# Kernel tuning notes

Hardware: AMD Instinct MI355X
Metric: run time of the kernel (lower is better)

The kernel has to match this reference:

```python
import jax, jax.numpy as jnp
import numpy as np

B, H, W, DIM, HEADS = 8, 128, 128, 256, 8
LH, LW = 8, 8
HD = DIM // HEADS
SCALE = HD ** -0.5
WS = LH * LW  # window size (tokens per window)


def setup_inputs() -> dict:
    key = jax.random.key(0)
    k1, k2, k3 = jax.random.split(key, 3)
    qkv = jax.random.normal(k1, (3, B, H * W, DIM), jnp.float32)
    lepe_w = jax.random.normal(k2, (DIM, 1, 3, 3), jnp.float32) * 0.1  # depthwise conv weight
    lepe_b = jax.random.normal(k3, (DIM,), jnp.float32) * 0.1
    return {"qkv": qkv, "lepe_w": lepe_w, "lepe_b": lepe_b}


def _to_local(x):
    # [B, L, C] -> [B*nH*nW, heads, LH*LW, head_dim]  (window partition)
    Bb, L, C = x.shape
    x = x.reshape(Bb, H // LH, LH, W // LW, LW, C).transpose(0, 1, 3, 2, 4, 5)
    x = x.reshape(-1, WS, HEADS, HD).transpose(0, 2, 1, 3)
    return x


def reference(qkv, lepe_w, lepe_b):
    q, k, v = qkv[0], qkv[1], qkv[2]
    Bb, L, C = q.shape
    q = _to_local(q) * SCALE            # [nWin, h, ws, d]
    k = _to_local(k)                    # [nWin, h, ws, d]
    # v windows in NCHW for depthwise LePE conv: [nWin, C, LH, LW]
    vw = v.reshape(Bb, H // LH, LH, W // LW, LW, C).transpose(0, 1, 3, 5, 2, 4)
    vw = vw.reshape(-1, C, LH, LW)
    lepe = jax.lax.conv_general_dilated(
        vw, lepe_w, window_strides=(1, 1), padding='SAME',
        feature_group_count=C,
        dimension_numbers=('NCHW', 'OIHW', 'NCHW')) + lepe_b[None, :, None, None]
    lepe = lepe.reshape(-1, HEADS, HD, WS).transpose(0, 1, 3, 2)   # [nWin, h, ws, d]
    vloc = vw.reshape(-1, HEADS, HD, WS).transpose(0, 1, 3, 2)     # [nWin, h, ws, d]
    attn = jax.nn.softmax(jnp.einsum('whqd,whkd->whqk', q, k), axis=-1)
    x = jnp.einsum('whqk,whkd->whqd', attn, vloc) + lepe           # [nWin, h, ws, d]
    # window merge back to [B, L, C]
    x = x.transpose(0, 2, 1, 3).reshape(-1, WS, C)
    x = x.reshape(Bb, H // LH, W // LW, LH, LW, C).transpose(0, 1, 3, 2, 4, 5)
    x = x.reshape(Bb, H * W, C)
    return x, q
```

## Files before the change

### kernel.cpp

```cpp
#include <hip/hip_runtime.h>
#include <hip/hip_bf16.h>


#define SCALE_F 0.17677669529663687f

typedef __attribute__((ext_vector_type(8))) short bf16x8;
typedef __attribute__((ext_vector_type(4))) float f32x4;

static __device__ __forceinline__ unsigned short f2bf(float f) {
    unsigned int u = __builtin_bit_cast(unsigned int, f);
    u += 0x7fffu + ((u >> 16) & 1u);
    return (unsigned short)(u >> 16);
}
static __device__ __forceinline__ float bf2f(unsigned short s) {
    unsigned int u = ((unsigned int)s) << 16;
    return __builtin_bit_cast(float, u);
}

__global__ __launch_bounds__(256) void lepe_attn_kernel(
    const float* __restrict__ qkv,
    const float* __restrict__ lw,
    const float* __restrict__ lb,
    float* __restrict__ out)
{
    const int bid  = blockIdx.x;
    const int head = bid & 7;
    const int win  = bid >> 3;
    const int ww   = win & 15;
    const int wh   = (win >> 4) & 15;
    const int b    = win >> 8;
    const int t    = threadIdx.x;

    __shared__ __align__(16) short q_hi[64][40];
    __shared__ __align__(16) short q_lo[64][40];
    __shared__ __align__(16) short k_hi[64][40];
    __shared__ __align__(16) short k_lo[64][40];
    __shared__ __align__(16) short v_t[32][72];
    __shared__ __align__(16) short P_lds[64][72];
    __shared__ float w_s[288];
    __shared__ float b_s[32];

    const float* Qp = qkv;
    const float* Kp = qkv + (size_t)33554432;
    const float* Vp = qkv + (size_t)67108864;
    float* xout = out;
    float* qout = out + (size_t)33554432;

    for (int i = t; i < 288; i += 256) w_s[i] = lw[head * 288 + i];
    if (t < 32) b_s[t] = lb[head * 32 + t];

    #pragma unroll
    for (int u = 0; u < 2; ++u) {
        const int idx = t + u * 256;
        const int s   = idx >> 3;
        const int d4  = idx & 7;
        const int row = wh * 8 + (s >> 3);
        const int col = ww * 8 + (s & 7);
        const size_t goff = ((size_t)(b * 16384 + row * 128 + col)) * 256
                          + head * 32 + d4 * 4;

        float4 fq = *(const float4*)(Qp + goff);
        fq.x *= SCALE_F; fq.y *= SCALE_F; fq.z *= SCALE_F; fq.w *= SCALE_F;
        *(float4*)(qout + ((size_t)bid * 64 + s) * 32 + d4 * 4) = fq;
        {
            unsigned short h0 = f2bf(fq.x), h1 = f2bf(fq.y),
                           h2 = f2bf(fq.z), h3 = f2bf(fq.w);
            unsigned short l0 = f2bf(fq.x - bf2f(h0)), l1 = f2bf(fq.y - bf2f(h1)),
                           l2 = f2bf(fq.z - bf2f(h2)), l3 = f2bf(fq.w - bf2f(h3));
            uint2 hp, lp;
            hp.x = (unsigned)h0 | ((unsigned)h1 << 16);
            hp.y = (unsigned)h2 | ((unsigned)h3 << 16);
            lp.x = (unsigned)l0 | ((unsigned)l1 << 16);
            lp.y = (unsigned)l2 | ((unsigned)l3 << 16);
            *(uint2*)&q_hi[s][d4 * 4] = hp;
            *(uint2*)&q_lo[s][d4 * 4] = lp;
        }
        {
            float4 fk = *(const float4*)(Kp + goff);
            unsigned short h0 = f2bf(fk.x), h1 = f2bf(fk.y),
                           h2 = f2bf(fk.z), h3 = f2bf(fk.w);
            unsigned short l0 = f2bf(fk.x - bf2f(h0)), l1 = f2bf(fk.y - bf2f(h1)),
                           l2 = f2bf(fk.z - bf2f(h2)), l3 = f2bf(fk.w - bf2f(h3));
            uint2 hp, lp;
            hp.x = (unsigned)h0 | ((unsigned)h1 << 16);
            hp.y = (unsigned)h2 | ((unsigned)h3 << 16);
            lp.x = (unsigned)l0 | ((unsigned)l1 << 16);
            lp.y = (unsigned)l2 | ((unsigned)l3 << 16);
            *(uint2*)&k_hi[s][d4 * 4] = hp;
            *(uint2*)&k_lo[s][d4 * 4] = lp;
        }
        {
            float4 fv = *(const float4*)(Vp + goff);
            const int sp = ((s & 15) << 2) | (s >> 4);
            v_t[d4 * 4 + 0][sp] = (short)f2bf(fv.x);
            v_t[d4 * 4 + 1][sp] = (short)f2bf(fv.y);
            v_t[d4 * 4 + 2][sp] = (short)f2bf(fv.z);
            v_t[d4 * 4 + 3][sp] = (short)f2bf(fv.w);
        }
    }
    __syncthreads();

    const int lane = t & 63;
    const int wid  = t >> 6;
    const int c    = lane & 15;
    const int g    = lane >> 4;
    const int i0   = wid * 16;

    bf16x8 aqh = *(const bf16x8*)&q_hi[i0 + c][g * 8];
    bf16x8 aql = *(const bf16x8*)&q_lo[i0 + c][g * 8];

    f32x4 sacc[4];
    #pragma unroll
    for (int jt = 0; jt < 4; ++jt) {
        bf16x8 bkh = *(const bf16x8*)&k_hi[jt * 16 + c][g * 8];
        bf16x8 bkl = *(const bf16x8*)&k_lo[jt * 16 + c][g * 8];
        f32x4 acc = {0.f, 0.f, 0.f, 0.f};
        acc = __builtin_amdgcn_mfma_f32_16x16x32_bf16(aqh, bkh, acc, 0, 0, 0);
        acc = __builtin_amdgcn_mfma_f32_16x16x32_bf16(aql, bkh, acc, 0, 0, 0);
        acc = __builtin_amdgcn_mfma_f32_16x16x32_bf16(aqh, bkl, acc, 0, 0, 0);
        sacc[jt] = acc;
    }

    float mx[4] = {-3.0e38f, -3.0e38f, -3.0e38f, -3.0e38f};
    #pragma unroll
    for (int jt = 0; jt < 4; ++jt)
        #pragma unroll
        for (int r = 0; r < 4; ++r)
            mx[r] = fmaxf(mx[r], sacc[jt][r]);
    #pragma unroll
    for (int r = 0; r < 4; ++r) {
        mx[r] = fmaxf(mx[r], __shfl_xor(mx[r], 1));
        mx[r] = fmaxf(mx[r], __shfl_xor(mx[r], 2));
        mx[r] = fmaxf(mx[r], __shfl_xor(mx[r], 4));
        mx[r] = fmaxf(mx[r], __shfl_xor(mx[r], 8));
    }
    float p[4][4];
    float sm[4] = {0.f, 0.f, 0.f, 0.f};
    #pragma unroll
    for (int jt = 0; jt < 4; ++jt)
        #pragma unroll
        for (int r = 0; r < 4; ++r) {
            p[jt][r] = __expf(sacc[jt][r] - mx[r]);
            sm[r] += p[jt][r];
        }
    #pragma unroll
    for (int r = 0; r < 4; ++r) {
        sm[r] += __shfl_xor(sm[r], 1);
        sm[r] += __shfl_xor(sm[r], 2);
        sm[r] += __shfl_xor(sm[r], 4);
        sm[r] += __shfl_xor(sm[r], 8);
    }
    #pragma unroll
    for (int r = 0; r < 4; ++r) {
        const float inv = 1.0f / sm[r];
        unsigned short b0 = f2bf(p[0][r] * inv);
        unsigned short b1 = f2bf(p[1][r] * inv);
        unsigned short b2 = f2bf(p[2][r] * inv);
        unsigned short b3 = f2bf(p[3][r] * inv);
        uint2 pk;
        pk.x = (unsigned)b0 | ((unsigned)b1 << 16);
        pk.y = (unsigned)b2 | ((unsigned)b3 << 16);
        *(uint2*)&P_lds[i0 + 4 * g + r][4 * c] = pk;
    }
    __syncthreads();

    f32x4 o0 = {0.f, 0.f, 0.f, 0.f};
    f32x4 o1 = {0.f, 0.f, 0.f, 0.f};
    #pragma unroll
    for (int ks = 0; ks < 2; ++ks) {
        bf16x8 pa  = *(const bf16x8*)&P_lds[i0 + c][ks * 32 + g * 8];
        bf16x8 vb0 = *(const bf16x8*)&v_t[c][ks * 32 + g * 8];
        bf16x8 vb1 = *(const bf16x8*)&v_t[16 + c][ks * 32 + g * 8];
        o0 = __builtin_amdgcn_mfma_f32_16x16x32_bf16(pa, vb0, o0, 0, 0, 0);
        o1 = __builtin_amdgcn_mfma_f32_16x16x32_bf16(pa, vb1, o1, 0, 0, 0);
    }
    __syncthreads();

    {
        const int td = t & 31;
        const int lh = t >> 5;
        float wv[9];
        #pragma unroll
        for (int k = 0; k < 9; ++k) wv[k] = w_s[td * 9 + k];
        float rv[3][8];
        #pragma unroll
        for (int dy = 0; dy < 3; ++dy) {
            const int r2 = lh + dy - 1;
            #pragma unroll
            for (int x = 0; x < 8; ++x) {
                if (r2 >= 0 && r2 < 8) {
                    const int s  = r2 * 8 + x;
                    const int sp = ((s & 15) << 2) | (s >> 4);
                    rv[dy][x] = bf2f((unsigned short)v_t[td][sp]);
                } else {
                    rv[dy][x] = 0.f;
                }
            }
        }
        float* lepe = (float*)P_lds;
        #pragma unroll
        for (int lwp = 0; lwp < 8; ++lwp) {
            float acc = b_s[td];
            #pragma unroll
            for (int dy = 0; dy < 3; ++dy)
                #pragma unroll
                for (int dx = 0; dx < 3; ++dx) {
                    const int x = lwp + dx - 1;
                    if (x >= 0 && x < 8) acc += wv[dy * 3 + dx] * rv[dy][x];
                }
            lepe[(lh * 8 + lwp) * 36 + td] = acc;
        }
    }
    __syncthreads();

    {
        const float* lepe = (const float*)P_lds;
        #pragma unroll
        for (int r = 0; r < 4; ++r) {
            const int s   = i0 + 4 * g + r;
            const int row = wh * 8 + (s >> 3);
            const int col = ww * 8 + (s & 7);
            float* xo = xout + ((size_t)(b * 16384 + row * 128 + col)) * 256
                      + head * 32;
            xo[c]      = o0[r] + lepe[s * 36 + c];
            xo[16 + c] = o1[r] + lepe[s * 36 + 16 + c];
        }
    }
}

extern "C" void kernel_launch(void* const* d_in, const int* in_sizes, int n_in,
                              void* d_out, int out_size, void* d_ws, size_t ws_size,
                              hipStream_t stream) {
    (void)in_sizes; (void)n_in; (void)out_size; (void)d_ws; (void)ws_size;
    const float* qkv = (const float*)d_in[0];
    const float* lw  = (const float*)d_in[1];
    const float* lb  = (const float*)d_in[2];
    float* out = (float*)d_out;
    lepe_attn_kernel<<<dim3(16384), dim3(256), 0, stream>>>(qkv, lw, lb, out);
}
```

Baseline: 153.6 us.

## Keep softmax probabilities in registers and fuse LePE conv into attention output

QK^T is computed transposed (K as the A operand), so each lane holds a full query column and softmax reductions need only two cross-lane shuffles. The normalized probabilities are packed straight into MFMA A-operand registers, which removes the P round trip through LDS and two barriers. The depthwise conv is computed per lane in the MFMA output layout from a new row-major V copy and added to the accumulators, removing the final LDS staging and barriers. The hi/lo split now truncates instead of rounding, occupancy is hinted at 5 blocks per CU, and the V^T column permutation is changed to match the new P layout. This adds register pressure and a second V store in LDS.

```diff
diff --git a/kernel.cpp b/kernel.cpp
--- a/kernel.cpp
+++ b/kernel.cpp
@@ -1,23 +1,35 @@
 #include <hip/hip_runtime.h>
-#include <hip/hip_bf16.h>
 
 
 #define SCALE_F 0.17677669529663687f
 
 typedef __attribute__((ext_vector_type(8))) short bf16x8;
 typedef __attribute__((ext_vector_type(4))) float f32x4;
+typedef __attribute__((ext_vector_type(4))) unsigned int u32x4;
 
 static __device__ __forceinline__ unsigned short f2bf(float f) {
-    unsigned int u = __builtin_bit_cast(unsigned int, f);
+    unsigned u = __builtin_bit_cast(unsigned, f);
     u += 0x7fffu + ((u >> 16) & 1u);
     return (unsigned short)(u >> 16);
 }
 static __device__ __forceinline__ float bf2f(unsigned short s) {
-    unsigned int u = ((unsigned int)s) << 16;
+    unsigned u = ((unsigned)s) << 16;
     return __builtin_bit_cast(float, u);
 }
-
-__global__ __launch_bounds__(256) void lepe_attn_kernel(
+static __device__ __forceinline__ void split2(float a, float b,
+                                              unsigned &hi, unsigned &lo) {
+    unsigned ua = __builtin_bit_cast(unsigned, a);
+    unsigned ub = __builtin_bit_cast(unsigned, b);
+    unsigned ha = ua & 0xffff0000u;
+    unsigned hb = ub & 0xffff0000u;
+    float ra = a - __builtin_bit_cast(float, ha);
+    float rb = b - __builtin_bit_cast(float, hb);
+    hi = (ha >> 16) | hb;
+    lo = (__builtin_bit_cast(unsigned, ra) >> 16)
+       | (__builtin_bit_cast(unsigned, rb) & 0xffff0000u);
+}
+
+__global__ __launch_bounds__(256, 5) void lepe_attn_kernel(
     const float* __restrict__ qkv,
     const float* __restrict__ lw,
     const float* __restrict__ lb,
@@ -36,7 +48,7 @@
     __shared__ __align__(16) short k_hi[64][40];
     __shared__ __align__(16) short k_lo[64][40];
     __shared__ __align__(16) short v_t[32][72];
-    __shared__ __align__(16) short P_lds[64][72];
+    __shared__ __align__(16) short v_lin[64][36];
     __shared__ float w_s[288];
     __shared__ float b_s[32];
 
@@ -60,43 +72,35 @@
                           + head * 32 + d4 * 4;
 
         float4 fq = *(const float4*)(Qp + goff);
+        float4 fk = *(const float4*)(Kp + goff);
+        float4 fv = *(const float4*)(Vp + goff);
+
         fq.x *= SCALE_F; fq.y *= SCALE_F; fq.z *= SCALE_F; fq.w *= SCALE_F;
         *(float4*)(qout + ((size_t)bid * 64 + s) * 32 + d4 * 4) = fq;
-        {
-            unsigned short h0 = f2bf(fq.x), h1 = f2bf(fq.y),
-                           h2 = f2bf(fq.z), h3 = f2bf(fq.w);
-            unsigned short l0 = f2bf(fq.x - bf2f(h0)), l1 = f2bf(fq.y - bf2f(h1)),
-                           l2 = f2bf(fq.z - bf2f(h2)), l3 = f2bf(fq.w - bf2f(h3));
-            uint2 hp, lp;
-            hp.x = (unsigned)h0 | ((unsigned)h1 << 16);
-            hp.y = (unsigned)h2 | ((unsigned)h3 << 16);
-            lp.x = (unsigned)l0 | ((unsigned)l1 << 16);
-            lp.y = (unsigned)l2 | ((unsigned)l3 << 16);
-            *(uint2*)&q_hi[s][d4 * 4] = hp;
-            *(uint2*)&q_lo[s][d4 * 4] = lp;
-        }
-        {
-            float4 fk = *(const float4*)(Kp + goff);
-            unsigned short h0 = f2bf(fk.x), h1 = f2bf(fk.y),
-                           h2 = f2bf(fk.z), h3 = f2bf(fk.w);
-            unsigned short l0 = f2bf(fk.x - bf2f(h0)), l1 = f2bf(fk.y - bf2f(h1)),
-                           l2 = f2bf(fk.z - bf2f(h2)), l3 = f2bf(fk.w - bf2f(h3));
-            uint2 hp, lp;
-            hp.x = (unsigned)h0 | ((unsigned)h1 << 16);
-            hp.y = (unsigned)h2 | ((unsigned)h3 << 16);
-            lp.x = (unsigned)l0 | ((unsigned)l1 << 16);
-            lp.y = (unsigned)l2 | ((unsigned)l3 << 16);
-            *(uint2*)&k_hi[s][d4 * 4] = hp;
-            *(uint2*)&k_lo[s][d4 * 4] = lp;
-        }
-        {
-            float4 fv = *(const float4*)(Vp + goff);
-            const int sp = ((s & 15) << 2) | (s >> 4);
-            v_t[d4 * 4 + 0][sp] = (short)f2bf(fv.x);
-            v_t[d4 * 4 + 1][sp] = (short)f2bf(fv.y);
-            v_t[d4 * 4 + 2][sp] = (short)f2bf(fv.z);
-            v_t[d4 * 4 + 3][sp] = (short)f2bf(fv.w);
-        }
+
+        uint2 hp, lp;
+        split2(fq.x, fq.y, hp.x, lp.x);
+        split2(fq.z, fq.w, hp.y, lp.y);
+        *(uint2*)&q_hi[s][d4 * 4] = hp;
+        *(uint2*)&q_lo[s][d4 * 4] = lp;
+
+        split2(fk.x, fk.y, hp.x, lp.x);
+        split2(fk.z, fk.w, hp.y, lp.y);
+        *(uint2*)&k_hi[s][d4 * 4] = hp;
+        *(uint2*)&k_lo[s][d4 * 4] = lp;
+
+        const unsigned short b0 = f2bf(fv.x), b1 = f2bf(fv.y),
+                             b2 = f2bf(fv.z), b3 = f2bf(fv.w);
+        uint2 vp;
+        vp.x = (unsigned)b0 | ((unsigned)b1 << 16);
+        vp.y = (unsigned)b2 | ((unsigned)b3 << 16);
+        *(uint2*)&v_lin[s][d4 * 4] = vp;
+        const int sp = ((s >> 1) & 1) * 32 + ((s >> 2) & 3) * 8
+                     + (s & 1) * 4 + (s >> 4);
+        v_t[d4 * 4 + 0][sp] = (short)b0;
+        v_t[d4 * 4 + 1][sp] = (short)b1;
+        v_t[d4 * 4 + 2][sp] = (short)b2;
+        v_t[d4 * 4 + 3][sp] = (short)b3;
     }
     __syncthreads();
 
@@ -106,125 +110,113 @@
     const int g    = lane >> 4;
     const int i0   = wid * 16;
 
-    bf16x8 aqh = *(const bf16x8*)&q_hi[i0 + c][g * 8];
-    bf16x8 aql = *(const bf16x8*)&q_lo[i0 + c][g * 8];
-
+    const bf16x8 bqh = *(const bf16x8*)&q_hi[i0 + c][g * 8];
+    const bf16x8 bql = *(const bf16x8*)&q_lo[i0 + c][g * 8];
     f32x4 sacc[4];
     #pragma unroll
     for (int jt = 0; jt < 4; ++jt) {
-        bf16x8 bkh = *(const bf16x8*)&k_hi[jt * 16 + c][g * 8];
-        bf16x8 bkl = *(const bf16x8*)&k_lo[jt * 16 + c][g * 8];
+        const bf16x8 akh = *(const bf16x8*)&k_hi[jt * 16 + c][g * 8];
+        const bf16x8 akl = *(const bf16x8*)&k_lo[jt * 16 + c][g * 8];
         f32x4 acc = {0.f, 0.f, 0.f, 0.f};
-        acc = __builtin_amdgcn_mfma_f32_16x16x32_bf16(aqh, bkh, acc, 0, 0, 0);
-        acc = __builtin_amdgcn_mfma_f32_16x16x32_bf16(aql, bkh, acc, 0, 0, 0);
-        acc = __builtin_amdgcn_mfma_f32_16x16x32_bf16(aqh, bkl, acc, 0, 0, 0);
+        acc = __builtin_amdgcn_mfma_f32_16x16x32_bf16(akh, bqh, acc, 0, 0, 0);
+        acc = __builtin_amdgcn_mfma_f32_16x16x32_bf16(akl, bqh, acc, 0, 0, 0);
+        acc = __builtin_amdgcn_mfma_f32_16x16x32_bf16(akh, bql, acc, 0, 0, 0);
         sacc[jt] = acc;
     }
 
-    float mx[4] = {-3.0e38f, -3.0e38f, -3.0e38f, -3.0e38f};
+    float mx = -3.0e38f;
     #pragma unroll
     for (int jt = 0; jt < 4; ++jt)
         #pragma unroll
         for (int r = 0; r < 4; ++r)
-            mx[r] = fmaxf(mx[r], sacc[jt][r]);
+            mx = fmaxf(mx, sacc[jt][r]);
+    mx = fmaxf(mx, __shfl_xor(mx, 16));
+    mx = fmaxf(mx, __shfl_xor(mx, 32));
+
+    float p[4][4];
+    float sm = 0.f;
+    #pragma unroll
+    for (int jt = 0; jt < 4; ++jt)
+        #pragma unroll
+        for (int r = 0; r < 4; ++r) {
+            p[jt][r] = __expf(sacc[jt][r] - mx);
+            sm += p[jt][r];
+        }
+    sm += __shfl_xor(sm, 16);
+    sm += __shfl_xor(sm, 32);
+    const float inv = 1.0f / sm;
+
+    unsigned dwA[4], dwB[4];
     #pragma unroll
     for (int r = 0; r < 4; ++r) {
-        mx[r] = fmaxf(mx[r], __shfl_xor(mx[r], 1));
-        mx[r] = fmaxf(mx[r], __shfl_xor(mx[r], 2));
-        mx[r] = fmaxf(mx[r], __shfl_xor(mx[r], 4));
-        mx[r] = fmaxf(mx[r], __shfl_xor(mx[r], 8));
-    }
-    float p[4][4];
-    float sm[4] = {0.f, 0.f, 0.f, 0.f};
-    #pragma unroll
-    for (int jt = 0; jt < 4; ++jt)
-        #pragma unroll
-        for (int r = 0; r < 4; ++r) {
-            p[jt][r] = __expf(sacc[jt][r] - mx[r]);
-            sm[r] += p[jt][r];
-        }
-    #pragma unroll
-    for (int r = 0; r < 4; ++r) {
-        sm[r] += __shfl_xor(sm[r], 1);
-        sm[r] += __shfl_xor(sm[r], 2);
-        sm[r] += __shfl_xor(sm[r], 4);
-        sm[r] += __shfl_xor(sm[r], 8);
-    }
-    #pragma unroll
-    for (int r = 0; r < 4; ++r) {
-        const float inv = 1.0f / sm[r];
-        unsigned short b0 = f2bf(p[0][r] * inv);
-        unsigned short b1 = f2bf(p[1][r] * inv);
-        unsigned short b2 = f2bf(p[2][r] * inv);
-        unsigned short b3 = f2bf(p[3][r] * inv);
-        uint2 pk;
-        pk.x = (unsigned)b0 | ((unsigned)b1 << 16);
-        pk.y = (unsigned)b2 | ((unsigned)b3 << 16);
-        *(uint2*)&P_lds[i0 + 4 * g + r][4 * c] = pk;
-    }
-    __syncthreads();
+        dwA[r] = (unsigned)f2bf(p[0][r] * inv)
+               | ((unsigned)f2bf(p[1][r] * inv) << 16);
+        dwB[r] = (unsigned)f2bf(p[2][r] * inv)
+               | ((unsigned)f2bf(p[3][r] * inv) << 16);
+    }
+    const u32x4 w0 = {dwA[0], dwB[0], dwA[1], dwB[1]};
+    const u32x4 w1 = {dwA[2], dwB[2], dwA[3], dwB[3]};
+    const bf16x8 pa0 = __builtin_bit_cast(bf16x8, w0);
+    const bf16x8 pa1 = __builtin_bit_cast(bf16x8, w1);
 
     f32x4 o0 = {0.f, 0.f, 0.f, 0.f};
     f32x4 o1 = {0.f, 0.f, 0.f, 0.f};
-    #pragma unroll
-    for (int ks = 0; ks < 2; ++ks) {
-        bf16x8 pa  = *(const bf16x8*)&P_lds[i0 + c][ks * 32 + g * 8];
-        bf16x8 vb0 = *(const bf16x8*)&v_t[c][ks * 32 + g * 8];
-        bf16x8 vb1 = *(const bf16x8*)&v_t[16 + c][ks * 32 + g * 8];
-        o0 = __builtin_amdgcn_mfma_f32_16x16x32_bf16(pa, vb0, o0, 0, 0, 0);
-        o1 = __builtin_amdgcn_mfma_f32_16x16x32_bf16(pa, vb1, o1, 0, 0, 0);
-    }
-    __syncthreads();
-
     {
-        const int td = t & 31;
-        const int lh = t >> 5;
+        const bf16x8 vb00 = *(const bf16x8*)&v_t[c][g * 8];
+        const bf16x8 vb10 = *(const bf16x8*)&v_t[16 + c][g * 8];
+        const bf16x8 vb01 = *(const bf16x8*)&v_t[c][32 + g * 8];
+        const bf16x8 vb11 = *(const bf16x8*)&v_t[16 + c][32 + g * 8];
+        o0 = __builtin_amdgcn_mfma_f32_16x16x32_bf16(pa0, vb00, o0, 0, 0, 0);
+        o1 = __builtin_amdgcn_mfma_f32_16x16x32_bf16(pa0, vb10, o1, 0, 0, 0);
+        o0 = __builtin_amdgcn_mfma_f32_16x16x32_bf16(pa1, vb01, o0, 0, 0, 0);
+        o1 = __builtin_amdgcn_mfma_f32_16x16x32_bf16(pa1, vb11, o1, 0, 0, 0);
+    }
+
+    const int srow  = 2 * wid + (g >> 1);
+    const int scol0 = 4 * (g & 1);
+    #pragma unroll
+    for (int half = 0; half < 2; ++half) {
+        const int ch = c + 16 * half;
         float wv[9];
         #pragma unroll
-        for (int k = 0; k < 9; ++k) wv[k] = w_s[td * 9 + k];
-        float rv[3][8];
+        for (int k2 = 0; k2 < 9; ++k2) wv[k2] = w_s[ch * 9 + k2];
+        float patch[3][6];
         #pragma unroll
         for (int dy = 0; dy < 3; ++dy) {
-            const int r2 = lh + dy - 1;
+            const int rr  = srow + dy - 1;
+            const bool rok = (rr >= 0) && (rr < 8);
+            const int rcl = rok ? rr : 0;
             #pragma unroll
-            for (int x = 0; x < 8; ++x) {
-                if (r2 >= 0 && r2 < 8) {
-                    const int s  = r2 * 8 + x;
-                    const int sp = ((s & 15) << 2) | (s >> 4);
-                    rv[dy][x] = bf2f((unsigned short)v_t[td][sp]);
-                } else {
-                    rv[dy][x] = 0.f;
-                }
+            for (int dx = 0; dx < 6; ++dx) {
+                const int cc  = scol0 + dx - 1;
+                const bool cok = (cc >= 0) && (cc < 8);
+                const int ccl = cok ? cc : 0;
+                const float vv = bf2f((unsigned short)v_lin[rcl * 8 + ccl][ch]);
+                patch[dy][dx] = (rok && cok) ? vv : 0.f;
             }
         }
-        float* lepe = (float*)P_lds;
-        #pragma unroll
-        for (int lwp = 0; lwp < 8; ++lwp) {
-            float acc = b_s[td];
+        const float bb = b_s[ch];
+        #pragma unroll
+        for (int r = 0; r < 4; ++r) {
+            float a = bb;
             #pragma unroll
             for (int dy = 0; dy < 3; ++dy)
                 #pragma unroll
-                for (int dx = 0; dx < 3; ++dx) {
-                    const int x = lwp + dx - 1;
-                    if (x >= 0 && x < 8) acc += wv[dy * 3 + dx] * rv[dy][x];
-                }
-            lepe[(lh * 8 + lwp) * 36 + td] = acc;
+                for (int dx = 0; dx < 3; ++dx)
+                    a += wv[dy * 3 + dx] * patch[dy][r + dx];
+            if (half == 0) o0[r] += a; else o1[r] += a;
         }
     }
-    __syncthreads();
-
-    {
-        const float* lepe = (const float*)P_lds;
-        #pragma unroll
-        for (int r = 0; r < 4; ++r) {
-            const int s   = i0 + 4 * g + r;
-            const int row = wh * 8 + (s >> 3);
-            const int col = ww * 8 + (s & 7);
-            float* xo = xout + ((size_t)(b * 16384 + row * 128 + col)) * 256
-                      + head * 32;
-            xo[c]      = o0[r] + lepe[s * 36 + c];
-            xo[16 + c] = o1[r] + lepe[s * 36 + 16 + c];
-        }
+
+    #pragma unroll
+    for (int r = 0; r < 4; ++r) {
+        const int s   = i0 + 4 * g + r;
+        const int row = wh * 8 + (s >> 3);
+        const int col = ww * 8 + (s & 7);
+        float* xo = xout + ((size_t)(b * 16384 + row * 128 + col)) * 256
+                  + head * 32;
+        xo[c]      = o0[r];
+        xo[16 + c] = o1[r];
     }
 }
 
```

After: 143.7 us. 6.4% less time.
